# Performance work log

Hardware: AMD Instinct MI355X
Metric: run time of the kernel (lower is better)

The kernel has to match this reference:

```python
import jax, jax.numpy as jnp
import numpy as np

B, L_ENC, L_DEC, PRED_LEN = 16, 720, 144, 96
D_MODEL, N_HEADS, D_FF, M_FEAT = 512, 8, 2048, 256
ENC_IN, DEC_IN, C_OUT, MARK = 7, 7, 7, 4
E_LAYERS = 2
DH = D_MODEL // N_HEADS


def _orf(m, d, seed):
    # Gaussian orthogonal random features (FAVOR+), scaling=0 (chi-norm rows).
    rng = np.random.default_rng(seed)
    blocks = [np.linalg.qr(rng.standard_normal((d, d)))[0].T for _ in range(m // d)]
    mat = np.concatenate(blocks, 0)  # [m, d]
    mult = np.linalg.norm(rng.standard_normal((m, d)), axis=1)
    return jnp.asarray(mult[:, None] * mat, dtype=jnp.float32)

PROJ_ENC = [_orf(M_FEAT, DH, s) for s in range(E_LAYERS)]
PROJ_DEC_SELF = _orf(M_FEAT, DH, 10)
PROJ_DEC_CROSS = _orf(M_FEAT, DH, 11)


def _pos_emb(n, d):
    pos = np.arange(n, dtype=np.float32)[:, None]
    div = np.exp(np.arange(0, d, 2, dtype=np.float32) * (-np.log(10000.0) / d))
    pe = np.zeros((n, d), dtype=np.float32)
    pe[:, 0::2] = np.sin(pos * div)
    pe[:, 1::2] = np.cos(pos * div)
    return jnp.asarray(pe)

PE_ENC = _pos_emb(L_ENC, D_MODEL)
PE_DEC = _pos_emb(L_DEC, D_MODEL)


def layer_norm(x, g, b):
    mu = x.mean(-1, keepdims=True)
    var = ((x - mu) ** 2).mean(-1, keepdims=True)
    return (x - mu) / jnp.sqrt(var + 1e-5) * g + b


def feature_map(x, proj, is_query):
    # FAVOR+ positive softmax kernel. x: [b,h,n,dh], proj: [m,dh]
    norm = DH ** -0.25
    xd = jnp.einsum('bhnd,md->bhnm', x * norm, proj)
    diag = (x ** 2).sum(-1) * (0.5 * norm * norm)  # [b,h,n]
    if is_query:
        stab = jax.lax.stop_gradient(xd.max(axis=-1, keepdims=True))
    else:
        stab = jax.lax.stop_gradient(xd.max(axis=(-1, -2), keepdims=True))
    return (M_FEAT ** -0.5) * (jnp.exp(xd - diag[..., None] - stab) + 1e-4)


def noncausal_attn(q, k, v):
    kv = jnp.einsum('bhnm,bhnd->bhmd', k, v)
    d_inv = 1.0 / jnp.einsum('bhnm,bhm->bhn', q, k.sum(2))
    return jnp.einsum('bhnm,bhmd,bhn->bhnd', q, kv, d_inv)


def causal_attn(q, k, v):
    # prefix-sum linear attention; carry S [b,h,m,dh], s [b,h,m]
    b, h, n, m = q.shape
    dh = v.shape[-1]

    def step(carry, qkv):
        S, s = carry
        qn, kn, vn = qkv
        S = S + kn[..., None] * vn[..., None, :]
        s = s + kn
        num = jnp.einsum('bhm,bhmd->bhd', qn, S)
        den = jnp.einsum('bhm,bhm->bh', qn, s)
        return (S, s), num / (den[..., None] + 1e-6)

    init = (jnp.zeros((b, h, m, dh), q.dtype), jnp.zeros((b, h, m), q.dtype))
    _, out = jax.lax.scan(step, init, (jnp.moveaxis(q, 2, 0), jnp.moveaxis(k, 2, 0), jnp.moveaxis(v, 2, 0)))
    return jnp.moveaxis(out, 0, 2)


def attention(x, ctx, Wq, Wk, Wv, Wo, bo, proj, causal):
    b, n, _ = x.shape
    nc = ctx.shape[1]
    q = (x @ Wq).reshape(b, n, N_HEADS, DH).transpose(0, 2, 1, 3)
    k = (ctx @ Wk).reshape(b, nc, N_HEADS, DH).transpose(0, 2, 1, 3)
    v = (ctx @ Wv).reshape(b, nc, N_HEADS, DH).transpose(0, 2, 1, 3)
    qp = feature_map(q, proj, True)
    kp = feature_map(k, proj, False)
    o = causal_attn(qp, kp, v) if causal else noncausal_attn(qp, kp, v)
    o = o.transpose(0, 2, 1, 3).reshape(b, n, D_MODEL)
    return o @ Wo + bo


def embed(x, mark, conv_w, time_w, pe):
    # TokenEmbedding: circular conv1d k=3 (no bias) + fixed sinusoidal PE + timeF linear
    xp = jnp.concatenate([x[:, -1:], x, x[:, :1]], axis=1)
    tok = (jnp.einsum('blc,cd->bld', xp[:, :-2], conv_w[0])
           + jnp.einsum('blc,cd->bld', xp[:, 1:-1], conv_w[1])
           + jnp.einsum('blc,cd->bld', xp[:, 2:], conv_w[2]))
    return tok + pe[None] + mark @ time_w


def _forward(x_enc, x_mark_enc, x_dec, x_mark_dec,
             emb_conv_enc, emb_time_enc, emb_conv_dec, emb_time_dec,
             enc_Wq, enc_Wk, enc_Wv, enc_Wo, enc_bo,
             enc_ff1, enc_b1, enc_ff2, enc_b2, enc_ln_g, enc_ln_b, enc_fg, enc_fb,
             dec_sWq, dec_sWk, dec_sWv, dec_sWo, dec_sbo,
             dec_cWq, dec_cWk, dec_cWv, dec_cWo, dec_cbo,
             dec_ff1, dec_b1, dec_ff2, dec_b2, dec_ln_g, dec_ln_b, dec_fg, dec_fb,
             proj_w, proj_b):
    gelu = lambda t: jax.nn.gelu(t, approximate=False)
    # RevIN-style instance normalization (means detached, as in the torch code)
    means = jax.lax.stop_gradient(x_enc.mean(1, keepdims=True))
    xc = x_enc - means
    stdev = jnp.sqrt(xc.var(1, keepdims=True) + 1e-5)
    xe = xc / stdev

    enc = embed(xe, x_mark_enc, emb_conv_enc, emb_time_enc, PE_ENC)
    for i in range(E_LAYERS):
        a = attention(enc, enc, enc_Wq[i], enc_Wk[i], enc_Wv[i], enc_Wo[i], enc_bo[i], PROJ_ENC[i], False)
        x1 = layer_norm(enc + a, enc_ln_g[i, 0], enc_ln_b[i, 0])
        y = gelu(x1 @ enc_ff1[i] + enc_b1[i]) @ enc_ff2[i] + enc_b2[i]
        enc = layer_norm(x1 + y, enc_ln_g[i, 1], enc_ln_b[i, 1])
    enc = layer_norm(enc, enc_fg, enc_fb)

    dec = embed(x_dec, x_mark_dec, emb_conv_dec, emb_time_dec, PE_DEC)
    a = attention(dec, dec, dec_sWq, dec_sWk, dec_sWv, dec_sWo, dec_sbo, PROJ_DEC_SELF, True)
    x1 = layer_norm(dec + a, dec_ln_g[0], dec_ln_b[0])
    c = attention(x1, enc, dec_cWq, dec_cWk, dec_cWv, dec_cWo, dec_cbo, PROJ_DEC_CROSS, False)
    x2 = layer_norm(x1 + c, dec_ln_g[1], dec_ln_b[1])
    y = gelu(x2 @ dec_ff1 + dec_b1) @ dec_ff2 + dec_b2
    dec = layer_norm(x2 + y, dec_ln_g[2], dec_ln_b[2])
    dec = layer_norm(dec, dec_fg, dec_fb)
    out = dec @ proj_w + proj_b  # [B, L_DEC, C_OUT]

    out = out * stdev[:, 0][:, None, :] + means[:, 0][:, None, :]
    return out[:, -PRED_LEN:, :]


def setup_inputs():
    ks = iter(jax.random.split(jax.random.key(0), 48))

    def rn(shape, scale=1.0):
        return jax.random.normal(next(ks), shape, dtype=jnp.float32) * scale

    w = 0.02
    E, D, F = E_LAYERS, D_MODEL, D_FF
    return {
        'x_enc': rn((B, L_ENC, ENC_IN)),
        'x_mark_enc': rn((B, L_ENC, MARK)),
        'x_dec': rn((B, L_DEC, DEC_IN)),
        'x_mark_dec': rn((B, L_DEC, MARK)),
        'emb_conv_enc': rn((3, ENC_IN, D), 0.1),
        'emb_time_enc': rn((MARK, D), w),
        'emb_conv_dec': rn((3, DEC_IN, D), 0.1),
        'emb_time_dec': rn((MARK, D), w),
        'enc_Wq': rn((E, D, D), w), 'enc_Wk': rn((E, D, D), w),
        'enc_Wv': rn((E, D, D), w), 'enc_Wo': rn((E, D, D), w),
        'enc_bo': jnp.zeros((E, D), jnp.float32),
        'enc_ff1': rn((E, D, F), w), 'enc_b1': jnp.zeros((E, F), jnp.float32),
        'enc_ff2': rn((E, F, D), w), 'enc_b2': jnp.zeros((E, D), jnp.float32),
        'enc_ln_g': jnp.ones((E, 2, D), jnp.float32), 'enc_ln_b': jnp.zeros((E, 2, D), jnp.float32),
        'enc_fg': jnp.ones((D,), jnp.float32), 'enc_fb': jnp.zeros((D,), jnp.float32),
        'dec_sWq': rn((D, D), w), 'dec_sWk': rn((D, D), w), 'dec_sWv': rn((D, D), w), 'dec_sWo': rn((D, D), w),
        'dec_sbo': jnp.zeros((D,), jnp.float32),
        'dec_cWq': rn((D, D), w), 'dec_cWk': rn((D, D), w), 'dec_cWv': rn((D, D), w), 'dec_cWo': rn((D, D), w),
        'dec_cbo': jnp.zeros((D,), jnp.float32),
        'dec_ff1': rn((D, F), w), 'dec_b1': jnp.zeros((F,), jnp.float32),
        'dec_ff2': rn((F, D), w), 'dec_b2': jnp.zeros((D,), jnp.float32),
        'dec_ln_g': jnp.ones((3, D), jnp.float32), 'dec_ln_b': jnp.zeros((3, D), jnp.float32),
        'dec_fg': jnp.ones((D,), jnp.float32), 'dec_fb': jnp.zeros((D,), jnp.float32),
        'proj_w': rn((D, C_OUT), w), 'proj_b': jnp.zeros((C_OUT,), jnp.float32),
    }


def reference(x_enc, x_mark_enc, x_dec, x_mark_dec,
              emb_conv_enc, emb_time_enc, emb_conv_dec, emb_time_dec,
              enc_Wq, enc_Wk, enc_Wv, enc_Wo, enc_bo,
              enc_ff1, enc_b1, enc_ff2, enc_b2, enc_ln_g, enc_ln_b, enc_fg, enc_fb,
              dec_sWq, dec_sWk, dec_sWv, dec_sWo, dec_sbo,
              dec_cWq, dec_cWk, dec_cWv, dec_cWo, dec_cbo,
              dec_ff1, dec_b1, dec_ff2, dec_b2, dec_ln_g, dec_ln_b, dec_fg, dec_fb,
              proj_w, proj_b):
    return _forward(x_enc, x_mark_enc, x_dec, x_mark_dec,
                    emb_conv_enc, emb_time_enc, emb_conv_dec, emb_time_dec,
                    enc_Wq, enc_Wk, enc_Wv, enc_Wo, enc_bo,
                    enc_ff1, enc_b1, enc_ff2, enc_b2, enc_ln_g, enc_ln_b, enc_fg, enc_fb,
                    dec_sWq, dec_sWk, dec_sWv, dec_sWo, dec_sbo,
                    dec_cWq, dec_cWk, dec_cWv, dec_cWo, dec_cbo,
                    dec_ff1, dec_b1, dec_ff2, dec_b2, dec_ln_g, dec_ln_b, dec_fg, dec_fb,
                    proj_w, proj_b)
```

## Files before the change

kernel.cpp:

```cpp
#include <hip/hip_runtime.h>
#include <math.h>
#include <string.h>

#define BB    16
#define LEc   720
#define LDc   144
#define PREDc 96
#define DMc   512
#define NHc   8
#define DHc   64
#define MFc   256
#define FFc   2048
#define NEc   (BB*LEc)
#define NDc   (BB*LDc)
#define BHc   (BB*NHc)
#define KSn   ((size_t)BHc*MFc)

typedef unsigned int u32;
typedef unsigned short u16;
typedef unsigned long long u64;
typedef unsigned __int128 u128;

typedef short bfx8 __attribute__((ext_vector_type(8)));
typedef float fx4  __attribute__((ext_vector_type(4)));
typedef unsigned short u16x4 __attribute__((ext_vector_type(4)));

struct NpSeedSeq {
  u32 pool[4];
  u32 hc;
  u32 hashmix(u32 v){ v ^= hc; hc *= 0x931e8875u; v *= hc; v ^= v >> 16; return v; }
  static u32 mixv(u32 x, u32 y){ u32 r = x*0xca01f9ddu - y*0x4973f715u; r ^= r >> 16; return r; }
  NpSeedSeq(u32 entropy){
    hc = 0x43b0d7e5u;
    for (int i=0;i<4;i++) pool[i] = hashmix(i==0 ? entropy : 0u);
    for (int s=0;s<4;s++)
      for (int d=0;d<4;d++)
        if (s!=d) pool[d] = mixv(pool[d], hashmix(pool[s]));
  }
  void generate8(u32* w){
    u32 h = 0x8b51f9ddu;
    for (int i=0;i<8;i++){
      u32 v = pool[i & 3];
      v ^= h; h *= 0x58f38dedu; v *= h; v ^= v >> 16;
      w[i] = v;
    }
  }
};

struct NpPCG64 {
  u128 state, inc;
  static u128 pcgmult(){ return ((u128)0x2360ed051fc65da4ull << 64) | 0x4385df649fccf645ull; }
  void step(){ state = state * pcgmult() + inc; }
  NpPCG64(u32 seed){
    NpSeedSeq ss(seed);
    u32 w[8]; ss.generate8(w);
    u64 v0 = (u64)w[0] | ((u64)w[1] << 32);
    u64 v1 = (u64)w[2] | ((u64)w[3] << 32);
    u64 v2 = (u64)w[4] | ((u64)w[5] << 32);
    u64 v3 = (u64)w[6] | ((u64)w[7] << 32);
    u128 initstate = ((u128)v0 << 64) | v1;
    u128 initseq   = ((u128)v2 << 64) | v3;
    state = 0; inc = (initseq << 1) | 1;
    step(); state += initstate; step();
  }
  u64 next64(){
    step();
    u64 hi = (u64)(state >> 64), lo = (u64)state;
    u32 rot = (u32)(state >> 122);
    u64 x = hi ^ lo;
    return (x >> rot) | (x << ((64u - rot) & 63u));
  }
  double nextDouble(){ return (double)(next64() >> 11) * (1.0/9007199254740992.0); }
};

static u64    zki[256];
static double zwi[256], zfi[256];
static void init_zig(){
  const double r  = 3.6541528853610087963519472518;
  const double mq = 4503599627370496.0;
  double fr = exp(-0.5*r*r);
  double vv = r*fr + sqrt(M_PI*0.5)*erfc(r/sqrt(2.0));
  double q  = vv/fr;
  zki[0] = (u64)((r/q)*mq);
  zki[1] = 0;
  zwi[0] = q/mq; zwi[255] = r/mq;
  zfi[0] = 1.0;  zfi[255] = fr;
  double tn = r, dn = r;
  for (int i=254;i>=1;i--){
    dn = sqrt(-2.0*log(vv/dn + exp(-0.5*dn*dn)));
    zki[i+1] = (u64)((dn/tn)*mq);
    tn = dn;
    zfi[i] = exp(-0.5*dn*dn);
    zwi[i] = dn/mq;
  }
}

static double std_normal(NpPCG64& g){
  const double nor_r = 3.6541528853610087963519472518;
  const double inv_r = 0.27366123732975827203338247596;
  for(;;){
    u64 rr = g.next64();
    int idx  = (int)(rr & 0xff); rr >>= 8;
    int sign = (int)(rr & 1);
    u64 rabs = (rr >> 1) & 0x000fffffffffffffULL;
    double x = (double)rabs * zwi[idx];
    if (sign) x = -x;
    if (rabs < zki[idx]) return x;
    if (idx == 0){
      double xx, yy;
      do {
        xx = -inv_r * log1p(-g.nextDouble());
        yy = -log1p(-g.nextDouble());
      } while (yy + yy <= xx*xx);
      return ((rabs >> 8) & 1) ? -(nor_r + xx) : (nor_r + xx);
    } else {
      if ((zfi[idx-1]-zfi[idx]) * g.nextDouble() + zfi[idx] < exp(-0.5*x*x)) return x;
    }
  }
}

static void qr_q64(double* A, double* Q){
  const int n = 64;
  static double V[64][64];
  static double tau[64];
  for (int j=0;j<n;j++){
    double alpha = A[j*n+j];
    double xn2 = 0;
    for (int i=j+1;i<n;i++) xn2 += A[i*n+j]*A[i*n+j];
    double xnorm = sqrt(xn2);
    if (xnorm == 0.0){
      tau[j] = 0.0;
      for (int i=j;i<n;i++) V[j][i] = (i==j) ? 1.0 : 0.0;
      continue;
    }
    double beta = -copysign(hypot(alpha, xnorm), alpha);
    double tj = (beta - alpha)/beta;
    double sc = 1.0/(alpha - beta);
    tau[j] = tj;
    V[j][j] = 1.0;
    for (int i=j+1;i<n;i++) V[j][i] = A[i*n+j]*sc;
    A[j*n+j] = beta;
    for (int c=j+1;c<n;c++){
      double w = 0;
      for (int i=j;i<n;i++) w += V[j][i]*A[i*n+c];
      w *= tj;
      for (int i=j;i<n;i++) A[i*n+c] -= V[j][i]*w;
    }
  }
  for (int i=0;i<n;i++) for (int c=0;c<n;c++) Q[i*n+c] = (i==c)?1.0:0.0;
  for (int j=n-1;j>=0;j--){
    double tj = tau[j];
    if (tj == 0.0) continue;
    for (int c=0;c<n;c++){
      double w = 0;
      for (int i=j;i<n;i++) w += V[j][i]*Q[i*n+c];
      w *= tj;
      for (int i=j;i<n;i++) Q[i*n+c] -= V[j][i]*w;
    }
  }
}

static void build_orf(u32 seed, float* outp){
  NpPCG64 g(seed);
  static double mat[MFc][DHc];
  static double A[64*64], Q[64*64];
  for (int blk=0; blk<4; blk++){
    for (int i=0;i<4096;i++) A[i] = std_normal(g);
    qr_q64(A, Q);
    for (int r=0;r<64;r++)
      for (int c=0;c<64;c++)
        mat[blk*64 + r][c] = Q[c*64 + r];
  }
  for (int r=0;r<MFc;r++){
    double ss = 0;
    double row[64];
    for (int c=0;c<64;c++){ row[c] = std_normal(g); ss += row[c]*row[c]; }
    double nrm = sqrt(ss);
    for (int c=0;c<64;c++) outp[r*64 + c] = (float)(nrm * mat[r][c]);
  }
}

static void build_all_proj(float* h){
  init_zig();
  const u32 seeds[4] = {0u, 1u, 10u, 11u};
  for (int s=0;s<4;s++) build_orf(seeds[s], h + (size_t)s*MFc*DHc);
}

__device__ __forceinline__ u16 f2bf(float x){
  u32 u = __builtin_bit_cast(u32, x);
  u32 r = (u + 0x7FFFu + ((u >> 16) & 1u)) >> 16;
  return (u16)r;
}
__device__ __forceinline__ float bf2f(u16 x){
  return __builtin_bit_cast(float, ((u32)x) << 16);
}


__global__ __launch_bounds__(256) void k_zero(float* __restrict__ p, int n){
  int i = blockIdx.x*256 + threadIdx.x;
  if (i < n) p[i] = 0.f;
}

__global__ __launch_bounds__(256) void k_projbf(const float* __restrict__ p, u16* __restrict__ pb, int n){
  int i = blockIdx.x*256 + threadIdx.x;
  if (i < n) pb[i] = f2bf(p[i]);
}

__global__ __launch_bounds__(256) void k_wtr(const float* __restrict__ W, u16* __restrict__ WT,
                                             int K, int N){
  __shared__ float t[32][33];
  int kb = blockIdx.x*32, nb = blockIdx.y*32;
  int tx = threadIdx.x & 31, ty = threadIdx.x >> 5;
  #pragma unroll
  for (int p=0;p<4;p++)
    t[ty + p*8][tx] = W[(size_t)(kb + ty + p*8)*N + nb + tx];
  __syncthreads();
  #pragma unroll
  for (int p=0;p<4;p++)
    WT[(size_t)(nb + ty + p*8)*K + kb + tx] = f2bf(t[tx][ty + p*8]);
}

__global__ __launch_bounds__(64) void k_meanstd(const float* __restrict__ x,
                                                float* __restrict__ means, float* __restrict__ stdev){
  int bc = blockIdx.x; int b = bc/7, c = bc%7;
  int t = threadIdx.x;
  float s=0;
  for (int l=t; l<LEc; l+=64) s += x[((size_t)b*LEc+l)*7 + c];
  for (int o=32;o;o>>=1) s += __shfl_down(s,o);
  s = __shfl(s,0);
  float mu = s / (float)LEc;
  float v=0;
  for (int l=t; l<LEc; l+=64){ float d = x[((size_t)b*LEc+l)*7+c]-mu; v += d*d; }
  for (int o=32;o;o>>=1) v += __shfl_down(v,o);
  if (t==0){ means[bc]=mu; stdev[bc]=sqrtf(v/(float)LEc + 1e-5f); }
}

__global__ __launch_bounds__(256) void k_embed(const float* __restrict__ x, const float* __restrict__ mark,
    const float* __restrict__ convw, const float* __restrict__ timew,
    const float* __restrict__ means, const float* __restrict__ stdev,
    int L, int donorm, float* __restrict__ outp)
{
  size_t idx = (size_t)blockIdx.x*256 + threadIdx.x;
  size_t total = (size_t)BB*L*DMc;
  if (idx >= total) return;
  int d = (int)(idx % DMc); size_t bl = idx / DMc; int l = (int)(bl % L); int b = (int)(bl / L);
  int lm = (l==0)? L-1 : l-1;
  int lp = (l==L-1)? 0 : l+1;
  int i2 = d & ~1;
  float div = expf((float)i2 * (-0.017988946039015984f));
  float ang = (float)l * div;
  float acc = (d & 1) ? cosf(ang) : sinf(ang);
  const float* xb = x + (size_t)b*L*7;
  #pragma unroll
  for (int c=0;c<7;c++){
    float v0 = xb[(size_t)lm*7+c], v1 = xb[(size_t)l*7+c], v2 = xb[(size_t)lp*7+c];
    if (donorm){
      float mu = means[b*7+c], sd = stdev[b*7+c];
      v0=(v0-mu)/sd; v1=(v1-mu)/sd; v2=(v2-mu)/sd;
    }
    acc += v0*convw[(0*7+c)*DMc+d] + v1*convw[(1*7+c)*DMc+d] + v2*convw[(2*7+c)*DMc+d];
  }
  const float* mb = mark + ((size_t)b*L + l)*4;
  #pragma unroll
  for (int t=0;t<4;t++) acc += mb[t]*timew[t*DMc+d];
  outp[idx] = acc;
}

template<int A_BF16, int OUT_BF16, int GELU>
__global__ __launch_bounds__(256) void k_gemm_mfma(
    const void* __restrict__ Ap, const u16* __restrict__ WT,
    const float* __restrict__ bias, void* __restrict__ Cp,
    int M, int N, int K)
{
  __shared__ u16 As[128][40];
  __shared__ u16 Bs[128][40];
  int nb = N >> 7;
  int bx = blockIdx.x % nb, by = blockIdx.x / nb;
  int row0 = by << 7, col0 = bx << 7;
  int tid = threadIdx.x;
  int wid = tid >> 6, lane = tid & 63;
  int wr = (wid >> 1) * 64, wc = (wid & 1) * 64;
  int l15 = lane & 15, lg = lane >> 4;
  fx4 acc[4][4];
  #pragma unroll
  for (int i=0;i<4;i++)
    #pragma unroll
    for (int j=0;j<4;j++)
      #pragma unroll
      for (int r=0;r<4;r++) acc[i][j][r] = 0.f;

  for (int k0 = 0; k0 < K; k0 += 32){
    if (A_BF16){
      const u16* A = (const u16*)Ap;
      #pragma unroll
      for (int p=0;p<2;p++){
        int idx = tid + (p<<8);
        int r = idx >> 2, kq = (idx & 3) << 3;
        *(bfx8*)&As[r][kq] = *(const bfx8*)(A + (size_t)(row0+r)*K + k0 + kq);
      }
    } else {
      const float* A = (const float*)Ap;
      #pragma unroll
      for (int p=0;p<4;p++){
        int idx = tid + (p<<8);
        int r = idx >> 3, kq = (idx & 7) << 2;
        float4 v = *(const float4*)(A + (size_t)(row0+r)*K + k0 + kq);
        u32 lo = (u32)f2bf(v.x) | ((u32)f2bf(v.y) << 16);
        u32 hi = (u32)f2bf(v.z) | ((u32)f2bf(v.w) << 16);
        *(u32*)&As[r][kq]   = lo;
        *(u32*)&As[r][kq+2] = hi;
      }
    }
    #pragma unroll
    for (int p=0;p<2;p++){
      int idx = tid + (p<<8);
      int c = idx >> 2, kq = (idx & 3) << 3;
      *(bfx8*)&Bs[c][kq] = *(const bfx8*)(WT + (size_t)(col0+c)*K + k0 + kq);
    }
    __syncthreads();
    int kg = lg << 3;
    bfx8 af[4], bf[4];
    #pragma unroll
    for (int i=0;i<4;i++) af[i] = *(const bfx8*)&As[wr + i*16 + l15][kg];
    #pragma unroll
    for (int j=0;j<4;j++) bf[j] = *(const bfx8*)&Bs[wc + j*16 + l15][kg];
    #pragma unroll
    for (int i=0;i<4;i++)
      #pragma unroll
      for (int j=0;j<4;j++)
        acc[i][j] = __builtin_amdgcn_mfma_f32_16x16x32_bf16(af[i], bf[j], acc[i][j], 0, 0, 0);
    __syncthreads();
  }
  #pragma unroll
  for (int j=0;j<4;j++){
    int col = col0 + wc + j*16 + l15;
    float bv = bias ? bias[col] : 0.f;
    #pragma unroll
    for (int i=0;i<4;i++){
      #pragma unroll
      for (int r=0;r<4;r++){
        int row = row0 + wr + i*16 + (lg<<2) + r;
        float v = acc[i][j][r] + bv;
        if (GELU) v = 0.5f*v*(1.0f + erff(v*0.7071067811865475f));
        if (OUT_BF16) ((u16*)Cp)[(size_t)row*N + col] = f2bf(v);
        else          ((float*)Cp)[(size_t)row*N + col] = v;
      }
    }
  }
}

static inline void gemm_bf(const void* A, const u16* WT, const float* bias, void* C,
                           int M, int N, int K, int abf, int obf, int gelu, hipStream_t st){
  dim3 g((N/128)*(M/128));
  if (abf)            k_gemm_mfma<1,0,0><<<g,256,0,st>>>(A,WT,bias,C,M,N,K);
  else if (gelu)      k_gemm_mfma<0,1,1><<<g,256,0,st>>>(A,WT,bias,C,M,N,K);
  else if (obf)       k_gemm_mfma<0,1,0><<<g,256,0,st>>>(A,WT,bias,C,M,N,K);
  else                k_gemm_mfma<0,0,0><<<g,256,0,st>>>(A,WT,bias,C,M,N,K);
}

__global__ __launch_bounds__(256) void k_rowmax_mfma(const u16* __restrict__ Kb,
    const u16* __restrict__ projbf, float* __restrict__ rowmax, int n)
{
  int ntile = n >> 4;
  int rt = blockIdx.x % ntile, bh = blockIdx.x / ntile;
  int b = bh >> 3, h = bh & 7;
  int row0 = rt << 4;
  int tid = threadIdx.x, w = tid >> 6, lane = tid & 63;
  int l15 = lane & 15, lg = lane >> 4;
  __shared__ u16 qs[16][72];
  __shared__ float xds[16][264];
  __shared__ float red[16][16];
  for (int i = tid; i < 16*16; i += 256){
    int r = i >> 4, dq = (i & 15)*4;
    *(u16x4*)&qs[r][dq] = *(const u16x4*)(Kb + ((size_t)b*n + row0 + r)*DMc + h*64 + dq);
  }
  __syncthreads();
  #pragma unroll
  for (int mt=0; mt<4; mt++){
    int m16 = (w*4+mt)*16;
    fx4 a2 = {0.f,0.f,0.f,0.f};
    #pragma unroll
    for (int ks=0; ks<2; ks++){
      bfx8 af = *(const bfx8*)&qs[l15][ks*32 + lg*8];
      bfx8 bf = *(const bfx8*)(projbf + (size_t)(m16+l15)*64 + ks*32 + lg*8);
      a2 = __builtin_amdgcn_mfma_f32_16x16x32_bf16(af, bf, a2, 0, 0, 0);
    }
    #pragma unroll
    for (int r=0;r<4;r++)
      xds[lg*4+r][m16+l15] = a2[r];
  }
  __syncthreads();
  { int r = tid >> 4, s = tid & 15;
    float mx = -1e30f;
    #pragma unroll
    for (int j=0;j<16;j++) mx = fmaxf(mx, xds[r][s*16+j]);
    red[r][s] = mx; }
  __syncthreads();
  if (tid < 16){
    float mx = -1e30f;
    #pragma unroll
    for (int j=0;j<16;j++) mx = fmaxf(mx, red[tid][j]);
    rowmax[(size_t)bh*n + row0 + tid] = mx * 0.35355339059327373f;
  }
}

__global__ __launch_bounds__(256) void k_stab(const float* __restrict__ rowmax, float* __restrict__ stab, int n){
  int bh = blockIdx.x; int tid = threadIdx.x;
  float mx = -1e30f;
  for (int i=tid;i<n;i+=256) mx = fmaxf(mx, rowmax[(size_t)bh*n+i]);
  __shared__ float red[4];
  for (int o=32;o;o>>=1) mx = fmaxf(mx, __shfl_xor(mx,o));
  if ((tid&63)==0) red[tid>>6]=mx;
  __syncthreads();
  if (tid==0) stab[bh] = fmaxf(fmaxf(red[0],red[1]),fmaxf(red[2],red[3]));
}

__global__ __launch_bounds__(256) void k_vtr(const u16* __restrict__ Vb, u16* __restrict__ Vt, int n){
  int nt = n >> 4;
  int blk = blockIdx.x; int t16 = blk % nt; int bh = blk / nt;
  int b = bh >> 3, h = bh & 7;
  int n0 = t16 << 4;
  int t = threadIdx.x;
  __shared__ u16 vt[16][72];
  { int r = t >> 4, d0 = (t & 15) * 4;
    *(u16x4*)&vt[r][d0] = *(const u16x4*)(Vb + ((size_t)b*n + n0 + r)*DMc + h*64 + d0); }
  __syncthreads();
  { int d = t >> 2, j = t & 3;
    u16x4 o;
    o.x = vt[j*4+0][d]; o.y = vt[j*4+1][d]; o.z = vt[j*4+2][d]; o.w = vt[j*4+3][d];
    *(u16x4*)(Vt + ((size_t)bh*64 + d)*(size_t)n + n0 + j*4) = o; }
}

__global__ __launch_bounds__(256) void k_kvfull(const u16* __restrict__ Kb,
    const u16* __restrict__ Vt, const u16* __restrict__ projbf, const float* __restrict__ stab,
    u16* __restrict__ KVT, float* __restrict__ KS, int n)
{
  int bh = blockIdx.x >> 1; int dh = (blockIdx.x & 1) * 32;
  int b = bh >> 3, h = bh & 7;
  int tid = threadIdx.x, w = tid >> 6, lane = tid & 63;
  int l15 = lane & 15, lg = lane >> 4;
  float sb = stab[bh];
  __shared__ u16 ksb[32][72];
  __shared__ u16 kpT[256][40];
  __shared__ u16 vsb[32][40];
  __shared__ float dgs[32];
  fx4 kv[2][4];
  #pragma unroll
  for (int i=0;i<2;i++)
    #pragma unroll
    for (int j=0;j<4;j++)
      #pragma unroll
      for (int r=0;r<4;r++) kv[i][j][r] = 0.f;
  float ksl[4] = {0.f,0.f,0.f,0.f};
  int nchunks = (n + 31) >> 5;
  for (int c=0; c<nchunks; c++){
    int n0 = c << 5;
    for (int i = tid; i < 32*16; i += 256){
      int r = i >> 4, dq = (i & 15) * 4;
      u16x4 v = {0,0,0,0};
      if (n0 + r < n) v = *(const u16x4*)(Kb + ((size_t)b*n + n0 + r)*DMc + h*64 + dq);
      *(u16x4*)&ksb[r][dq] = v;
    }
    for (int i = tid; i < 32*8; i += 256){
      int r = i >> 3, nq4 = (i & 7) * 4;
      u16x4 v = {0,0,0,0};
      const u16* src = Vt + ((size_t)bh*64 + dh + r)*(size_t)n + n0 + nq4;
      if (n0 + nq4 + 3 < n) v = *(const u16x4*)src;
      else { for (int j=0;j<4;j++) if (n0+nq4+j < n) v[j] = src[j]; }
      *(u16x4*)&vsb[r][nq4] = v;
    }
    __syncthreads();
    if (tid < 32){
      float dg = 0;
      #pragma unroll 16
      for (int d=0; d<64; d++){ float kd = bf2f(ksb[tid][d]); dg = fmaf(kd,kd,dg); }
      dgs[tid] = dg * 0.0625f;
    }
    __syncthreads();
    #pragma unroll
    for (int mt=0; mt<4; mt++){
      int m16 = (w*4 + mt)*16;
      #pragma unroll
      for (int nt=0; nt<2; nt++){
        fx4 a2 = {0.f,0.f,0.f,0.f};
        #pragma unroll
        for (int ks=0; ks<2; ks++){
          bfx8 af = *(const bfx8*)&ksb[nt*16 + l15][ks*32 + lg*8];
          bfx8 bf = *(const bfx8*)(projbf + (size_t)(m16 + l15)*64 + ks*32 + lg*8);
          a2 = __builtin_amdgcn_mfma_f32_16x16x32_bf16(af, bf, a2, 0, 0, 0);
        }
        #pragma unroll
        for (int r=0;r<4;r++){
          int nn = nt*16 + lg*4 + r;
          float kp = 0.f;
          if (n0 + nn < n)
            kp = (expf(a2[r]*0.35355339059327373f - dgs[nn] - sb) + 1e-4f) * 0.0625f;
          ksl[mt] += kp;
          kpT[m16 + l15][nn] = f2bf(kp);
        }
      }
    }
    __syncthreads();
    #pragma unroll
    for (int dt=0; dt<2; dt++){
      #pragma unroll
      for (int mt=0; mt<4; mt++){
        bfx8 af = *(const bfx8*)&vsb[dt*16 + l15][lg*8];
        bfx8 bf = *(const bfx8*)&kpT[(w*4+mt)*16 + l15][lg*8];
        kv[dt][mt] = __builtin_amdgcn_mfma_f32_16x16x32_bf16(af, bf, kv[dt][mt], 0, 0, 0);
      }
    }
    __syncthreads();
  }
  if (dh == 0){
    #pragma unroll
    for (int mt=0; mt<4; mt++){
      float v = ksl[mt];
      v += __shfl_xor(v, 16);
      v += __shfl_xor(v, 32);
      if (lg == 0) KS[(size_t)bh*MFc + (w*4+mt)*16 + l15] = v;
    }
  }
  #pragma unroll
  for (int dt=0; dt<2; dt++)
    #pragma unroll
    for (int mt=0; mt<4; mt++)
      #pragma unroll
      for (int r=0;r<4;r++){
        int d = dh + dt*16 + lg*4 + r;
        int m = (w*4+mt)*16 + l15;
        KVT[((size_t)bh*64 + d)*MFc + m] = f2bf(kv[dt][mt][r]);
      }
}

__global__ __launch_bounds__(256) void k_attn_mfma(const u16* __restrict__ Qb,
    const u16* __restrict__ projbf, const u16* __restrict__ KVT, const float* __restrict__ KS,
    u16* __restrict__ O, int nq)
{
  int ntile = nq >> 4;
  int rt = blockIdx.x % ntile, bh = blockIdx.x / ntile;
  int b = bh >> 3, h = bh & 7;
  int row0 = rt << 4;
  int tid = threadIdx.x, w = tid >> 6, lane = tid & 63;
  int l15 = lane & 15, lg = lane >> 4;
  __shared__ u16 qs[16][72];
  __shared__ float xds[16][264];
  __shared__ u16 qpl[16][264];
  __shared__ float dgs[16], mxs[16], dns[16];
  __shared__ float red[16][16];
  __shared__ float kss[256];
  for (int i = tid; i < 16*16; i += 256){
    int r = i >> 4, dq = (i & 15)*4;
    *(u16x4*)&qs[r][dq] = *(const u16x4*)(Qb + ((size_t)b*nq + row0 + r)*DMc + h*64 + dq);
  }
  kss[tid] = KS[(size_t)bh*MFc + tid];
  __syncthreads();
  if (tid < 16){
    float dg = 0;
    #pragma unroll 16
    for (int d=0;d<64;d++){ float q = bf2f(qs[tid][d]); dg = fmaf(q,q,dg); }
    dgs[tid] = dg * 0.0625f;
  }
  #pragma unroll
  for (int mt=0; mt<4; mt++){
    int m16 = (w*4+mt)*16;
    fx4 a2 = {0.f,0.f,0.f,0.f};
    #pragma unroll
    for (int ks=0; ks<2; ks++){
      bfx8 af = *(const bfx8*)&qs[l15][ks*32 + lg*8];
      bfx8 bf = *(const bfx8*)(projbf + (size_t)(m16+l15)*64 + ks*32 + lg*8);
      a2 = __builtin_amdgcn_mfma_f32_16x16x32_bf16(af, bf, a2, 0, 0, 0);
    }
    #pragma unroll
    for (int r=0;r<4;r++)
      xds[lg*4+r][m16+l15] = a2[r]*0.35355339059327373f;
  }
  __syncthreads();
  { int r = tid >> 4, s = tid & 15;
    float mx = -1e30f;
    #pragma unroll
    for (int j=0;j<16;j++) mx = fmaxf(mx, xds[r][s*16+j]);
    red[r][s] = mx; }
  __syncthreads();
  if (tid < 16){
    float mx = -1e30f;
    #pragma unroll
    for (int j=0;j<16;j++) mx = fmaxf(mx, red[tid][j]);
    mxs[tid] = mx;
  }
  __syncthreads();
  { int r = tid >> 4, s = tid & 15;
    float dg = dgs[r], mx = mxs[r], pd = 0;
    #pragma unroll
    for (int j=0;j<16;j++){
      int m = s*16+j;
      float v = (expf(xds[r][m] - dg - mx) + 1e-4f)*0.0625f;
      qpl[r][m] = f2bf(v);
      pd = fmaf(v, kss[m], pd);
    }
    red[r][s] = pd; }
  __syncthreads();
  if (tid < 16){
    float s = 0;
    #pragma unroll
    for (int j=0;j<16;j++) s += red[tid][j];
    dns[tid] = 1.0f / s;
  }
  __syncthreads();
  fx4 a2 = {0.f,0.f,0.f,0.f};
  #pragma unroll
  for (int ks=0; ks<8; ks++){
    bfx8 af = *(const bfx8*)&qpl[l15][ks*32 + lg*8];
    bfx8 bf = *(const bfx8*)(KVT + ((size_t)bh*64 + w*16 + l15)*MFc + ks*32 + lg*8);
    a2 = __builtin_amdgcn_mfma_f32_16x16x32_bf16(af, bf, a2, 0, 0, 0);
  }
  #pragma unroll
  for (int r=0;r<4;r++){
    int row = lg*4 + r;
    O[((size_t)b*nq + row0 + row)*DMc + h*64 + w*16 + l15] = f2bf(a2[r]*dns[row]);
  }
}

template<int ISQ>
__global__ __launch_bounds__(256) void k_fmap_mfma(const u16* __restrict__ Xb,
    const u16* __restrict__ projbf, const float* __restrict__ stab,
    u16* __restrict__ P, int n)
{
  int ntile = n >> 4;
  int rt = blockIdx.x % ntile, bh = blockIdx.x / ntile;
  int b = bh >> 3, h = bh & 7;
  int row0 = rt << 4;
  int tid = threadIdx.x, w = tid >> 6, lane = tid & 63;
  int l15 = lane & 15, lg = lane >> 4;
  __shared__ u16 qs[16][72];
  __shared__ float xds[16][264];
  __shared__ float dgs[16], mxs[16];
  __shared__ float red[16][16];
  for (int i = tid; i < 16*16; i += 256){
    int r = i >> 4, dq = (i & 15)*4;
    *(u16x4*)&qs[r][dq] = *(const u16x4*)(Xb + ((size_t)b*n + row0 + r)*DMc + h*64 + dq);
  }
  __syncthreads();
  if (tid < 16){
    float dg = 0;
    #pragma unroll 16
    for (int d=0;d<64;d++){ float q = bf2f(qs[tid][d]); dg = fmaf(q,q,dg); }
    dgs[tid] = dg * 0.0625f;
  }
  #pragma unroll
  for (int mt=0; mt<4; mt++){
    int m16 = (w*4+mt)*16;
    fx4 a2 = {0.f,0.f,0.f,0.f};
    #pragma unroll
    for (int ks=0; ks<2; ks++){
      bfx8 af = *(const bfx8*)&qs[l15][ks*32 + lg*8];
      bfx8 bf = *(const bfx8*)(projbf + (size_t)(m16+l15)*64 + ks*32 + lg*8);
      a2 = __builtin_amdgcn_mfma_f32_16x16x32_bf16(af, bf, a2, 0, 0, 0);
    }
    #pragma unroll
    for (int r=0;r<4;r++)
      xds[lg*4+r][m16+l15] = a2[r]*0.35355339059327373f;
  }
  __syncthreads();
  if (ISQ){
    { int r = tid >> 4, s = tid & 15;
      float mx = -1e30f;
      #pragma unroll
      for (int j=0;j<16;j++) mx = fmaxf(mx, xds[r][s*16+j]);
      red[r][s] = mx; }
    __syncthreads();
    if (tid < 16){
      float mx = -1e30f;
      #pragma unroll
      for (int j=0;j<16;j++) mx = fmaxf(mx, red[tid][j]);
      mxs[tid] = mx;
    }
    __syncthreads();
  }
  { int r = tid >> 4, s = tid & 15;
    float sv = ISQ ? mxs[r] : stab[bh];
    float dg = dgs[r];
    u16* dst = P + ((size_t)bh*n + row0 + r)*MFc;
    #pragma unroll
    for (int j=0;j<16;j++){
      int m = s*16+j;
      dst[m] = f2bf((expf(xds[r][m] - dg - sv) + 1e-4f)*0.0625f);
    }
  }
}

__global__ __launch_bounds__(256) void k_causal_mfma(const u16* __restrict__ PQ,
    const u16* __restrict__ PK, const u16* __restrict__ Vt, u16* __restrict__ O, int n)
{
  int ntile = n >> 4;
  int it = blockIdx.x % ntile, bh = blockIdx.x / ntile;
  int b = bh >> 3, h = bh & 7;
  int row0 = it << 4;
  int tid = threadIdx.x, w = tid >> 6, lane = tid & 63;
  int l15 = lane & 15, lg = lane >> 4;
  __shared__ u16 qp[16][264];
  __shared__ float sf[16][168];
  __shared__ u16 sb[16][168];
  __shared__ u16 vt[64][168];
  __shared__ float dns[16];
  __shared__ float red[16][16];
  #pragma unroll
  for (int p=0;p<4;p++){
    int idx = tid + (p<<8);
    int r = idx >> 6, c4 = (idx & 63)*4;
    *(u16x4*)&qp[r][c4] = *(const u16x4*)(PQ + ((size_t)bh*n + row0 + r)*MFc + c4);
  }
  for (int i = tid; i < 64*40; i += 256){
    int r = i / 40, c4 = (i % 40)*4;
    u16x4 v = {0,0,0,0};
    if (c4 < 144) v = *(const u16x4*)(Vt + ((size_t)bh*64 + r)*(size_t)n + c4);
    *(u16x4*)&vt[r][c4] = v;
  }
  { int r = tid >> 4, c = 144 + (tid & 15);
    sb[r][c] = 0; sf[r][c] = 0.f; }
  __syncthreads();
  for (int jt = w; jt < 9; jt += 4){
    fx4 a2 = {0.f,0.f,0.f,0.f};
    #pragma unroll
    for (int ks=0; ks<8; ks++){
      bfx8 af = *(const bfx8*)&qp[l15][ks*32 + lg*8];
      bfx8 bf = *(const bfx8*)(PK + ((size_t)bh*n + jt*16 + l15)*MFc + ks*32 + lg*8);
      a2 = __builtin_amdgcn_mfma_f32_16x16x32_bf16(af, bf, a2, 0, 0, 0);
    }
    int jg = jt*16 + l15;
    #pragma unroll
    for (int r=0;r<4;r++){
      int il = lg*4 + r;
      float v = (jg <= row0 + il) ? a2[r] : 0.f;
      sf[il][jg] = v;
      sb[il][jg] = f2bf(v);
    }
  }
  __syncthreads();
  { int r = tid >> 4, s = tid & 15;
    float pd = 0;
    #pragma unroll
    for (int q=0;q<9;q++) pd += sf[r][s*9 + q];
    red[r][s] = pd; }
  __syncthreads();
  if (tid < 16){
    float s = 0;
    #pragma unroll
    for (int j=0;j<16;j++) s += red[tid][j];
    dns[tid] = 1.0f / (s + 1e-6f);
  }
  __syncthreads();
  fx4 a2 = {0.f,0.f,0.f,0.f};
  #pragma unroll
  for (int ks=0; ks<5; ks++){
    bfx8 af = *(const bfx8*)&sb[l15][ks*32 + lg*8];
    bfx8 bf = *(const bfx8*)&vt[w*16 + l15][ks*32 + lg*8];
    a2 = __builtin_amdgcn_mfma_f32_16x16x32_bf16(af, bf, a2, 0, 0, 0);
  }
  #pragma unroll
  for (int r=0;r<4;r++){
    int il = lg*4 + r;
    O[((size_t)b*n + row0 + il)*DMc + h*64 + w*16 + l15] = f2bf(a2[r]*dns[il]);
  }
}

__global__ __launch_bounds__(128) void k_ln(const float* __restrict__ A, const float* __restrict__ Bres,
    const float* __restrict__ g, const float* __restrict__ beta, float* __restrict__ outp)
{
  size_t row = blockIdx.x; int t = threadIdx.x;
  float4 v = *(const float4*)(A + row*DMc + t*4);
  if (Bres){ float4 w = *(const float4*)(Bres + row*DMc + t*4); v.x+=w.x; v.y+=w.y; v.z+=w.z; v.w+=w.w; }
  __shared__ float red[2];
  float s = v.x+v.y+v.z+v.w;
  for (int o=32;o;o>>=1) s += __shfl_xor(s,o);
  if ((t&63)==0) red[t>>6]=s;
  __syncthreads();
  float mu = (red[0]+red[1]) * (1.0f/DMc);
  float dx=v.x-mu, dy=v.y-mu, dz=v.z-mu, dw=v.w-mu;
  float qq = dx*dx+dy*dy+dz*dz+dw*dw;
  __syncthreads();
  for (int o=32;o;o>>=1) qq += __shfl_xor(qq,o);
  if ((t&63)==0) red[t>>6]=qq;
  __syncthreads();
  float var = (red[0]+red[1]) * (1.0f/DMc);
  float rs = 1.0f / sqrtf(var + 1e-5f);
  const float4 g4 = *(const float4*)(g + t*4);
  const float4 b4 = *(const float4*)(beta + t*4);
  float4 o4;
  o4.x = dx*rs*g4.x + b4.x;
  o4.y = dy*rs*g4.y + b4.y;
  o4.z = dz*rs*g4.z + b4.z;
  o4.w = dw*rs*g4.w + b4.w;
  *(float4*)(outp + row*DMc + t*4) = o4;
}

__global__ __launch_bounds__(64) void k_final(const float* __restrict__ X, const float* __restrict__ pw,
   const float* __restrict__ pb, const float* __restrict__ means, const float* __restrict__ stdev,
   float* __restrict__ outp)
{
  int blk = blockIdx.x; int lo = blk % PREDc; int b = blk / PREDc;
  int l = lo + (LDc - PREDc);
  int t = threadIdx.x;
  float acc[7];
  #pragma unroll
  for (int c=0;c<7;c++) acc[c]=0;
  const float* xr = X + ((size_t)b*LDc + l)*DMc;
  for (int d=t; d<DMc; d+=64){
    float xv = xr[d];
    #pragma unroll
    for (int c=0;c<7;c++) acc[c] = fmaf(xv, pw[d*7+c], acc[c]);
  }
  #pragma unroll
  for (int c=0;c<7;c++){
    float s = acc[c];
    for (int o=32;o;o>>=1) s += __shfl_xor(s,o);
    if (t==0)
      outp[((size_t)b*PREDc + lo)*7 + c] = (s + pb[c]) * stdev[b*7+c] + means[b*7+c];
  }
}

extern "C" void kernel_launch(void* const* d_in, const int* in_sizes, int n_in,
                              void* d_out, int out_size, void* d_ws, size_t ws_size,
                              hipStream_t stream)
{
  (void)in_sizes; (void)n_in;
  const float* x_enc        = (const float*)d_in[0];
  const float* x_mark_enc   = (const float*)d_in[1];
  const float* x_dec        = (const float*)d_in[2];
  const float* x_mark_dec   = (const float*)d_in[3];
  const float* emb_conv_enc = (const float*)d_in[4];
  const float* emb_time_enc = (const float*)d_in[5];
  const float* emb_conv_dec = (const float*)d_in[6];
  const float* emb_time_dec = (const float*)d_in[7];
  const float* enc_Wq = (const float*)d_in[8];
  const float* enc_Wk = (const float*)d_in[9];
  const float* enc_Wv = (const float*)d_in[10];
  const float* enc_Wo = (const float*)d_in[11];
  const float* enc_bo = (const float*)d_in[12];
  const float* enc_ff1 = (const float*)d_in[13];
  const float* enc_b1  = (const float*)d_in[14];
  const float* enc_ff2 = (const float*)d_in[15];
  const float* enc_b2  = (const float*)d_in[16];
  const float* enc_ln_g = (const float*)d_in[17];
  const float* enc_ln_b = (const float*)d_in[18];
  const float* enc_fg = (const float*)d_in[19];
  const float* enc_fb = (const float*)d_in[20];
  const float* dec_sWq = (const float*)d_in[21];
  const float* dec_sWk = (const float*)d_in[22];
  const float* dec_sWv = (const float*)d_in[23];
  const float* dec_sWo = (const float*)d_in[24];
  const float* dec_sbo = (const float*)d_in[25];
  const float* dec_cWq = (const float*)d_in[26];
  const float* dec_cWk = (const float*)d_in[27];
  const float* dec_cWv = (const float*)d_in[28];
  const float* dec_cWo = (const float*)d_in[29];
  const float* dec_cbo = (const float*)d_in[30];
  const float* dec_ff1 = (const float*)d_in[31];
  const float* dec_b1  = (const float*)d_in[32];
  const float* dec_ff2 = (const float*)d_in[33];
  const float* dec_b2  = (const float*)d_in[34];
  const float* dec_ln_g = (const float*)d_in[35];
  const float* dec_ln_b = (const float*)d_in[36];
  const float* dec_fg = (const float*)d_in[37];
  const float* dec_fb = (const float*)d_in[38];
  const float* proj_w = (const float*)d_in[39];
  const float* proj_b = (const float*)d_in[40];
  float* outp = (float*)d_out;
  float* W = (float*)d_ws;

  size_t o = 0;
  #define ALLOCF(nm, n) size_t nm = o; o += (((size_t)(n)) + 63) & ~(size_t)63;
  ALLOCF(o_proj, 4*MFc*DHc)
  ALLOCF(o_projbf, 2*MFc*DHc)
  ALLOCF(o_means, BB*7)
  ALLOCF(o_std,   BB*7)
  ALLOCF(o_rmE, (size_t)BHc*LEc)
  ALLOCF(o_rmD, (size_t)BHc*LDc)
  ALLOCF(o_stab, BHc)
  ALLOCF(o_KS, KSn)
  ALLOCF(o_Dx1, (size_t)NDc*DMc)
  ALLOCF(o_WT, 5242880)
  ALLOCF(o_Xb, (size_t)NEc*DMc)
  ALLOCF(o_X1, (size_t)NEc*DMc)
  ALLOCF(o_U,  11796480)
  #undef ALLOCF
  size_t needed_bytes = o * sizeof(float);
  if (ws_size < needed_bytes){
    k_zero<<<(out_size+255)/256, 256, 0, stream>>>(outp, out_size);
    return;
  }

  float* Xb  = W + o_Xb;
  float* X1  = W + o_X1;
  float* KS  = W + o_KS;
  float* rmE = W + o_rmE;
  float* rmD = W + o_rmD;
  float* stb = W + o_stab;
  u16*  WTb = (u16*)(W + o_WT);
  u16*  Uh  = (u16*)(W + o_U);
  u16*  PJB = (u16*)(W + o_projbf);

  const size_t NEu = (size_t)NEc*DMc;
  const size_t NDu = (size_t)NDc*DMc;
  u16* Tq = Uh;            u16* Tk = Uh + NEu;
  u16* Tv = Uh + 2*NEu;    u16* Oe = Uh + 3*NEu;
  u16* FFb = Uh;
  u16*   VtU  = (u16*)X1;
  u16*   KVTu = (u16*)(X1 + 2949120);
  u16* dTq = Uh;           u16* dTk = Uh + NDu;
  u16* dTv = Uh + 2*NDu;   u16* dOd = Uh + 3*NDu;
  u16* PQb = Uh + 4*NDu;
  u16* PKb = PQb + (size_t)BHc*LDc*MFc;
  u16* VtD = PKb + (size_t)BHc*LDc*MFc;
  u16* cTk = Uh;           u16* cTv = Uh + NEu;
  u16* dTq2 = Uh + 2*NEu;  u16* cOd = Uh + 2*NEu + NDu;
  u16* dFF = Uh;
  float* DX  = X1 + 0*NDu;
  float* Da  = X1 + 1*NDu;
  float* Dx2 = X1 + 2*NDu;
  float* Dy  = X1 + 3*NDu;
  float* Dx1 = W + o_Dx1;

  static float h_proj[4*MFc*DHc];
  build_all_proj(h_proj);
  hipMemcpyAsync(W + o_proj, h_proj, sizeof(h_proj), hipMemcpyHostToDevice, stream);
  k_projbf<<<(4*MFc*DHc)/256, 256, 0, stream>>>(W + o_proj, PJB, 4*MFc*DHc);
  const u16* pb_enc0  = PJB + 0*MFc*DHc;
  const u16* pb_enc1  = PJB + 1*MFc*DHc;
  const u16* pb_self  = PJB + 2*MFc*DHc;
  const u16* pb_cross = PJB + 3*MFc*DHc;

  size_t wto = 0;
  auto xpose = [&](const float* Wsrc, int K, int N) -> const u16* {
    u16* dst = WTb + wto; wto += (size_t)K*N;
    k_wtr<<<dim3(K/32, N/32), 256, 0, stream>>>(Wsrc, dst, K, N);
    return dst;
  };
  const u16 *wQ[2], *wK[2], *wV[2], *wO[2], *wF1[2], *wF2[2];
  for (int i=0;i<2;i++){
    wQ[i]  = xpose(enc_Wq + (size_t)i*DMc*DMc, DMc, DMc);
    wK[i]  = xpose(enc_Wk + (size_t)i*DMc*DMc, DMc, DMc);
    wV[i]  = xpose(enc_Wv + (size_t)i*DMc*DMc, DMc, DMc);
    wO[i]  = xpose(enc_Wo + (size_t)i*DMc*DMc, DMc, DMc);
    wF1[i] = xpose(enc_ff1 + (size_t)i*DMc*FFc, DMc, FFc);
    wF2[i] = xpose(enc_ff2 + (size_t)i*FFc*DMc, FFc, DMc);
  }
  const u16* wsQ = xpose(dec_sWq, DMc, DMc);
  const u16* wsK = xpose(dec_sWk, DMc, DMc);
  const u16* wsV = xpose(dec_sWv, DMc, DMc);
  const u16* wsO = xpose(dec_sWo, DMc, DMc);
  const u16* wcQ = xpose(dec_cWq, DMc, DMc);
  const u16* wcK = xpose(dec_cWk, DMc, DMc);
  const u16* wcV = xpose(dec_cWv, DMc, DMc);
  const u16* wcO = xpose(dec_cWo, DMc, DMc);
  const u16* wdF1 = xpose(dec_ff1, DMc, FFc);
  const u16* wdF2 = xpose(dec_ff2, FFc, DMc);

  auto kv_chain = [&](const u16* Kbuf, const u16* Vbuf, const u16* pjb){
    k_rowmax_mfma<<<BHc*(LEc/16), 256, 0, stream>>>(Kbuf, pjb, rmE, LEc);
    k_stab<<<BHc, 256, 0, stream>>>(rmE, stb, LEc);
    k_vtr<<<BHc*(LEc/16), 256, 0, stream>>>(Vbuf, VtU, LEc);
    k_kvfull<<<BHc*2, 256, 0, stream>>>(Kbuf, VtU, pjb, stb, KVTu, KS, LEc);
  };

  k_meanstd<<<BB*7, 64, 0, stream>>>(x_enc, W+o_means, W+o_std);
  k_embed<<<(BB*LEc*DMc)/256, 256, 0, stream>>>(x_enc, x_mark_enc, emb_conv_enc, emb_time_enc,
                                                W+o_means, W+o_std, LEc, 1, Xb);

  for (int i=0;i<2;i++){
    const float* bo = enc_bo + (size_t)i*DMc;
    const float* b1 = enc_b1  + (size_t)i*FFc;
    const float* b2 = enc_b2  + (size_t)i*DMc;
    const float* g0 = enc_ln_g + (size_t)(i*2+0)*DMc;
    const float* e0 = enc_ln_b + (size_t)(i*2+0)*DMc;
    const float* g1 = enc_ln_g + (size_t)(i*2+1)*DMc;
    const float* e1 = enc_ln_b + (size_t)(i*2+1)*DMc;
    const u16*   pjb = (i==0) ? pb_enc0 : pb_enc1;

    gemm_bf(Xb, wQ[i], nullptr, Tq, NEc, DMc, DMc, 0,1,0, stream);
    gemm_bf(Xb, wK[i], nullptr, Tk, NEc, DMc, DMc, 0,1,0, stream);
    gemm_bf(Xb, wV[i], nullptr, Tv, NEc, DMc, DMc, 0,1,0, stream);
    kv_chain(Tk, Tv, pjb);
    k_attn_mfma<<<BHc*(LEc/16), 256, 0, stream>>>(Tq, pjb, KVTu, KS, Oe, LEc);
    gemm_bf(Oe, wO[i], bo, X1, NEc, DMc, DMc, 1,0,0, stream);
    k_ln<<<NEc, 128, 0, stream>>>(X1, Xb, g0, e0, X1);
    gemm_bf(X1, wF1[i], b1, FFb, NEc, FFc, DMc, 0,1,1, stream);
    gemm_bf(FFb, wF2[i], b2, Xb, NEc, DMc, FFc, 1,0,0, stream);
    k_ln<<<NEc, 128, 0, stream>>>(Xb, X1, g1, e1, Xb);
  }
  k_ln<<<NEc, 128, 0, stream>>>(Xb, nullptr, enc_fg, enc_fb, Xb);

  k_embed<<<(BB*LDc*DMc)/256, 256, 0, stream>>>(x_dec, x_mark_dec, emb_conv_dec, emb_time_dec,
                                                W+o_means, W+o_std, LDc, 0, DX);
  gemm_bf(DX, wsQ, nullptr, dTq, NDc, DMc, DMc, 0,1,0, stream);
  gemm_bf(DX, wsK, nullptr, dTk, NDc, DMc, DMc, 0,1,0, stream);
  gemm_bf(DX, wsV, nullptr, dTv, NDc, DMc, DMc, 0,1,0, stream);
  k_rowmax_mfma<<<BHc*(LDc/16), 256, 0, stream>>>(dTk, pb_self, rmD, LDc);
  k_stab<<<BHc, 256, 0, stream>>>(rmD, stb, LDc);
  k_fmap_mfma<1><<<BHc*(LDc/16), 256, 0, stream>>>(dTq, pb_self, nullptr, PQb, LDc);
  k_fmap_mfma<0><<<BHc*(LDc/16), 256, 0, stream>>>(dTk, pb_self, stb, PKb, LDc);
  k_vtr<<<BHc*(LDc/16), 256, 0, stream>>>(dTv, VtD, LDc);
  k_causal_mfma<<<BHc*(LDc/16), 256, 0, stream>>>(PQb, PKb, VtD, dOd, LDc);
  gemm_bf(dOd, wsO, dec_sbo, Da, NDc, DMc, DMc, 1,0,0, stream);
  k_ln<<<NDc, 128, 0, stream>>>(Da, DX, dec_ln_g + 0*DMc, dec_ln_b + 0*DMc, Dx1);

  gemm_bf(Dx1, wcQ, nullptr, dTq2, NDc, DMc, DMc, 0,1,0, stream);
  gemm_bf(Xb,  wcK, nullptr, cTk,  NEc, DMc, DMc, 0,1,0, stream);
  gemm_bf(Xb,  wcV, nullptr, cTv,  NEc, DMc, DMc, 0,1,0, stream);
  kv_chain(cTk, cTv, pb_cross);
  k_attn_mfma<<<BHc*(LDc/16), 256, 0, stream>>>(dTq2, pb_cross, KVTu, KS, cOd, LDc);
  gemm_bf(cOd, wcO, dec_cbo, Da, NDc, DMc, DMc, 1,0,0, stream);
  k_ln<<<NDc, 128, 0, stream>>>(Da, Dx1, dec_ln_g + 1*DMc, dec_ln_b + 1*DMc, Dx2);

  gemm_bf(Dx2, wdF1, dec_b1, dFF, NDc, FFc, DMc, 0,1,1, stream);
  gemm_bf(dFF, wdF2, dec_b2, Dy, NDc, DMc, FFc, 1,0,0, stream);
  k_ln<<<NDc, 128, 0, stream>>>(Dy, Dx2, dec_ln_g + 2*DMc, dec_ln_b + 2*DMc, Da);
  k_ln<<<NDc, 128, 0, stream>>>(Da, nullptr, dec_fg, dec_fb, Da);
  k_final<<<BB*PREDc, 64, 0, stream>>>(Da, proj_w, proj_b, W+o_means, W+o_std, outp);
}
```

Before: 1.519 ms.

## Split KV accumulation over sequence into three partial slabs and reduce

The k_kvfull kernel previously launched only 256 blocks, each walking the full encoder sequence serially. It now splits the sequence chunks three ways, so three times as many blocks run, each writing partial KV and key-sum results to separate slabs. A new k_kvred3 kernel then sums the three slabs. The per-chunk diagonal norm computation is also spread across all threads with a shuffle reduction instead of 32 serial threads. The cost is an extra launch, extra memory traffic, and bf16 rounding of the partials before they are summed.

```diff
diff --git a/kernel.cpp b/kernel.cpp
--- a/kernel.cpp
+++ b/kernel.cpp
@@ -15,6 +15,7 @@
 #define NDc   (BB*LDc)
 #define BHc   (BB*NHc)
 #define KSn   ((size_t)BHc*MFc)
+#define KVTn  ((size_t)BHc*64*MFc)
 
 typedef unsigned int u32;
 typedef unsigned short u16;
@@ -433,9 +434,12 @@
 
 __global__ __launch_bounds__(256) void k_kvfull(const u16* __restrict__ Kb,
     const u16* __restrict__ Vt, const u16* __restrict__ projbf, const float* __restrict__ stab,
-    u16* __restrict__ KVT, float* __restrict__ KS, int n)
+    u16* __restrict__ KVP, float* __restrict__ KSP, int n)
 {
-  int bh = blockIdx.x >> 1; int dh = (blockIdx.x & 1) * 32;
+  int blk = blockIdx.x;
+  int ns = blk % 3;
+  int rest = blk / 3;
+  int bh = rest >> 1; int dh = (rest & 1) * 32;
   int b = bh >> 3, h = bh & 7;
   int tid = threadIdx.x, w = tid >> 6, lane = tid & 63;
   int l15 = lane & 15, lg = lane >> 4;
@@ -453,7 +457,10 @@
       for (int r=0;r<4;r++) kv[i][j][r] = 0.f;
   float ksl[4] = {0.f,0.f,0.f,0.f};
   int nchunks = (n + 31) >> 5;
-  for (int c=0; c<nchunks; c++){
+  int cper = (nchunks + 2) / 3;
+  int c0 = ns * cper;
+  int c1 = c0 + cper; if (c1 > nchunks) c1 = nchunks;
+  for (int c=c0; c<c1; c++){
     int n0 = c << 5;
     for (int i = tid; i < 32*16; i += 256){
       int r = i >> 4, dq = (i & 15) * 4;
@@ -470,11 +477,13 @@
       *(u16x4*)&vsb[r][nq4] = v;
     }
     __syncthreads();
-    if (tid < 32){
+    {
+      int r = tid >> 3, j = tid & 7;
       float dg = 0;
-      #pragma unroll 16
-      for (int d=0; d<64; d++){ float kd = bf2f(ksb[tid][d]); dg = fmaf(kd,kd,dg); }
-      dgs[tid] = dg * 0.0625f;
+      #pragma unroll
+      for (int q=0;q<8;q++){ float kd = bf2f(ksb[r][j*8+q]); dg = fmaf(kd,kd,dg); }
+      dg += __shfl_down(dg,4); dg += __shfl_down(dg,2); dg += __shfl_down(dg,1);
+      if (j == 0) dgs[r] = dg * 0.0625f;
     }
     __syncthreads();
     #pragma unroll
@@ -518,9 +527,10 @@
       float v = ksl[mt];
       v += __shfl_xor(v, 16);
       v += __shfl_xor(v, 32);
-      if (lg == 0) KS[(size_t)bh*MFc + (w*4+mt)*16 + l15] = v;
-    }
-  }
+      if (lg == 0) KSP[(size_t)ns*KSn + (size_t)bh*MFc + (w*4+mt)*16 + l15] = v;
+    }
+  }
+  u16* slab = KVP + (size_t)ns*KVTn;
   #pragma unroll
   for (int dt=0; dt<2; dt++)
     #pragma unroll
@@ -529,8 +539,19 @@
       for (int r=0;r<4;r++){
         int d = dh + dt*16 + lg*4 + r;
         int m = (w*4+mt)*16 + l15;
-        KVT[((size_t)bh*64 + d)*MFc + m] = f2bf(kv[dt][mt][r]);
+        slab[((size_t)bh*64 + d)*MFc + m] = f2bf(kv[dt][mt][r]);
       }
+}
+
+__global__ __launch_bounds__(256) void k_kvred3(const u16* __restrict__ KVP, u16* __restrict__ KVT,
+    const float* __restrict__ KSP, float* __restrict__ KS)
+{
+  size_t i = (size_t)blockIdx.x*256 + threadIdx.x;
+  if (i < KVTn){
+    float s = bf2f(KVP[i]) + bf2f(KVP[KVTn + i]) + bf2f(KVP[2*KVTn + i]);
+    KVT[i] = f2bf(s);
+  }
+  if (i < KSn) KS[i] = KSP[i] + KSP[KSn + i] + KSP[2*KSn + i];
 }
 
 __global__ __launch_bounds__(256) void k_attn_mfma(const u16* __restrict__ Qb,
@@ -878,6 +899,7 @@
   ALLOCF(o_rmD, (size_t)BHc*LDc)
   ALLOCF(o_stab, BHc)
   ALLOCF(o_KS, KSn)
+  ALLOCF(o_KSP, 3*KSn)
   ALLOCF(o_Dx1, (size_t)NDc*DMc)
   ALLOCF(o_WT, 5242880)
   ALLOCF(o_Xb, (size_t)NEc*DMc)
@@ -893,6 +915,7 @@
   float* Xb  = W + o_Xb;
   float* X1  = W + o_X1;
   float* KS  = W + o_KS;
+  float* KSP = W + o_KSP;
   float* rmE = W + o_rmE;
   float* rmD = W + o_rmD;
   float* stb = W + o_stab;
@@ -907,6 +930,7 @@
   u16* FFb = Uh;
   u16*   VtU  = (u16*)X1;
   u16*   KVTu = (u16*)(X1 + 2949120);
+  u16*   KVPs = Uh + 2*NEu + 2*NDu;
   u16* dTq = Uh;           u16* dTk = Uh + NDu;
   u16* dTv = Uh + 2*NDu;   u16* dOd = Uh + 3*NDu;
   u16* PQb = Uh + 4*NDu;
@@ -960,7 +984,8 @@
     k_rowmax_mfma<<<BHc*(LEc/16), 256, 0, stream>>>(Kbuf, pjb, rmE, LEc);
     k_stab<<<BHc, 256, 0, stream>>>(rmE, stb, LEc);
     k_vtr<<<BHc*(LEc/16), 256, 0, stream>>>(Vbuf, VtU, LEc);
-    k_kvfull<<<BHc*2, 256, 0, stream>>>(Kbuf, VtU, pjb, stb, KVTu, KS, LEc);
+    k_kvfull<<<BHc*2*3, 256, 0, stream>>>(Kbuf, VtU, pjb, stb, KVPs, KSP, LEc);
+    k_kvred3<<<(int)((KVTn+255)/256), 256, 0, stream>>>(KVPs, KVTu, KSP, KS);
   };
 
   k_meanstd<<<BB*7, 64, 0, stream>>>(x_enc, W+o_means, W+o_std);
```

After: 3.859 ms. 154% more time.
